# Optimization experiments

Hardware: AMD Instinct MI355X
Metric: run time of the kernel (lower is better)

## Reference

```python
import jax, jax.numpy as jnp
import numpy as np

K = 10        # neighbors
SIGMA = 1.0   # gaussian bandwidth
BIG = 1e9     # diagonal fill so a point is never its own neighbor


def _knn_idx(h, k):
    # h: (B, T, H) -> idx: (B, T, k) of nearest neighbors (euclidean), excluding self
    # squared-distance trick avoids materializing (B, T, T, H)
    sq = jnp.sum(h * h, axis=-1)                                  # (B, T)
    d2 = sq[:, :, None] + sq[:, None, :] - 2.0 * jnp.einsum('bth,bsh->bts', h, h)
    d = jnp.sqrt(jnp.maximum(d2, 0.0))                            # (B, T, T)
    T = h.shape[1]
    eye = jnp.eye(T, dtype=bool)
    d = jnp.where(eye[None, :, :], BIG, d)
    k_eff = min(k, T - 1)
    _, idx = jax.lax.top_k(-d, k_eff)                             # smallest distances
    return idx


def setup_inputs() -> dict:
    key = jax.random.key(0)
    ks = jax.random.split(key, 5)
    B, T, C, H = 64, 1024, 64, 32
    x = jax.random.normal(ks[0], (B, T, C), dtype=jnp.float32)
    s1 = 1.0 / np.sqrt(C)
    s2 = 1.0 / np.sqrt(H)
    W1 = jax.random.uniform(ks[1], (C, H), minval=-s1, maxval=s1, dtype=jnp.float32)
    b1 = jax.random.uniform(ks[2], (H,), minval=-s1, maxval=s1, dtype=jnp.float32)
    W2 = jax.random.uniform(ks[3], (H, H), minval=-s2, maxval=s2, dtype=jnp.float32)
    b2 = jax.random.uniform(ks[4], (H,), minval=-s2, maxval=s2, dtype=jnp.float32)
    return {"x": x, "W1": W1, "b1": b1, "W2": W2, "b2": b2}


def reference(x, W1, b1, W2, b2):
    h = x @ W1 + b1                                               # (B, T, H)
    # kNN graph built under no_grad in the original
    idx = _knn_idx(jax.lax.stop_gradient(h), K)                   # (B, T, k)
    # gather neighbors without the (B, T, T, H) expansion
    neigh = jax.vmap(lambda hb, ib: hb[ib])(h, idx)               # (B, T, k, H)
    diff = neigh - h[:, :, None, :]
    dist = jnp.sqrt(jnp.sum(diff * diff, axis=-1))                # (B, T, k)
    w = jnp.exp(-dist ** 2 / (2.0 * SIGMA ** 2 + 1e-8))
    w = w / (jnp.sum(w, axis=-1, keepdims=True) + 1e-8)
    smooth = jnp.einsum('btk,btkh->bth', w, neigh)                # (B, T, H)
    lap = h - smooth
    return jnp.tanh(lap) @ W2 + b2
```

## Files before the change

### kernel.cpp

```cpp
#include <hip/hip_runtime.h>
#include <math.h>

#define BB 64
#define TT 1024
#define CC 64
#define HH 32
#define KNN 10

typedef float v4f __attribute__((ext_vector_type(4)));
typedef _Float16 f16x8 __attribute__((ext_vector_type(8)));

__device__ __forceinline__ unsigned umn(unsigned a, unsigned b) { return a < b ? a : b; }
__device__ __forceinline__ unsigned umx(unsigned a, unsigned b) { return a > b ? a : b; }

__global__ __launch_bounds__(256) void h_kernel(
    const float* __restrict__ x, const float* __restrict__ W1,
    const float* __restrict__ b1, float* __restrict__ h, float* __restrict__ hsq)
{
    __shared__ float w1s[CC][HH];
    __shared__ float b1s[HH];
    int tid = threadIdx.x;
    for (int i = tid; i < CC * HH; i += 256) w1s[i >> 5][i & 31] = W1[i];
    if (tid < HH) b1s[tid] = b1[tid];
    __syncthreads();

    int row = blockIdx.x * 256 + tid;
    const float4* xr = (const float4*)(x + (size_t)row * CC);
    float acc[HH];
    #pragma unroll
    for (int j = 0; j < HH; ++j) acc[j] = b1s[j];
    #pragma unroll
    for (int c4 = 0; c4 < CC / 4; ++c4) {
        float4 xv = xr[c4];
        #pragma unroll
        for (int j = 0; j < HH; ++j) {
            acc[j] = fmaf(xv.x, w1s[c4 * 4 + 0][j], acc[j]);
            acc[j] = fmaf(xv.y, w1s[c4 * 4 + 1][j], acc[j]);
            acc[j] = fmaf(xv.z, w1s[c4 * 4 + 2][j], acc[j]);
            acc[j] = fmaf(xv.w, w1s[c4 * 4 + 3][j], acc[j]);
        }
    }
    float s = 0.f;
    #pragma unroll
    for (int j = 0; j < HH; ++j) s = fmaf(acc[j], acc[j], s);
    float* hr = h + (size_t)row * HH;
    #pragma unroll
    for (int q = 0; q < HH / 4; ++q) {
        float4 v = { acc[4*q], acc[4*q+1], acc[4*q+2], acc[4*q+3] };
        ((float4*)hr)[q] = v;
    }
    hsq[row] = 0.5f * s * 1048576.0f;
}

#define INSERT_PAIR(kE, kO) do {                                       \
    unsigned lo_ = umn(kE, kO), hi_ = umx(kE, kO);                     \
    bd9 = umn(umn(bd9, umx(bd8, lo_)), umx(bd7, hi_));                 \
    bd8 = umn(umn(bd8, umx(bd7, lo_)), umx(bd6, hi_));                 \
    bd7 = umn(umn(bd7, umx(bd6, lo_)), umx(bd5, hi_));                 \
    bd6 = umn(umn(bd6, umx(bd5, lo_)), umx(bd4, hi_));                 \
    bd5 = umn(umn(bd5, umx(bd4, lo_)), umx(bd3, hi_));                 \
    bd4 = umn(umn(bd4, umx(bd3, lo_)), umx(bd2, hi_));                 \
    bd3 = umn(umn(bd3, umx(bd2, lo_)), umx(bd1, hi_));                 \
    bd2 = umn(umn(bd2, umx(bd1, lo_)), umx(bd0, hi_));                 \
    bd1 = umn(umn(bd1, umx(bd0, lo_)), hi_);                           \
    bd0 = umn(bd0, lo_);                                               \
} while (0)

__global__ __launch_bounds__(512, 8) void lap_kernel(
    const float* __restrict__ h, const float* __restrict__ hsq,
    const float* __restrict__ W2, const float* __restrict__ b2,
    float* __restrict__ out)
{
    __shared__ __align__(16) unsigned char smem[36864];
    auto cah  = reinterpret_cast<_Float16 (*)[2][64][32]>(smem);
    auto cal  = reinterpret_cast<_Float16 (*)[2][64][32]>(smem + 16384);
    float* hsql = reinterpret_cast<float*>(smem + 32768);
    auto s_key  = reinterpret_cast<unsigned (*)[64][KNN]>(smem);
    float* e_wk = reinterpret_cast<float*>(smem + 20480);
    short* e_id = reinterpret_cast<short*>(smem + 23040);
    float* e_inv = reinterpret_cast<float*>(smem + 24320);
    float* w2s  = reinterpret_cast<float*>(smem + 24576);
    float* b2s  = reinterpret_cast<float*>(smem + 28672);
    float* a_pool = reinterpret_cast<float*>(smem);

    int tid  = threadIdx.x;
    int lane = tid & 63;
    int wid  = __builtin_amdgcn_readfirstlane(tid >> 6);

    int g   = blockIdx.x;
    int l   = g >> 3;
    int bb  = ((g & 7) << 3) | (l & 7);
    int rb  = (l >> 3) << 6;

    const float* hb  = h   + (size_t)bb * TT * HH;
    const float* sqb = hsq + (size_t)bb * TT;

    int gtg  = wid & 3;
    int half = wid >> 2;
    int n    = lane & 15;
    int kc   = lane >> 4;

    int trow = rb + gtg * 16 + n;
    f16x8 Bhi, Blo;
    {
        const float* tp = hb + (size_t)trow * HH + kc * 8;
        float4 f1 = ((const float4*)tp)[0];
        float4 f2 = ((const float4*)tp)[1];
        float tf[8] = { f1.x, f1.y, f1.z, f1.w, f2.x, f2.y, f2.z, f2.w };
        #pragma unroll
        for (int e = 0; e < 8; ++e) {
            _Float16 hh = (_Float16)tf[e];
            Bhi[e] = hh;
            Blo[e] = (_Float16)(tf[e] - (float)hh);
        }
    }
    float cinit20 = sqb[trow] + 1048576.0f;

    int s_local = trow - half * 512;
    bool selfok = ((unsigned)s_local < 512u) && (((s_local >> 2) & 3) == kc);
    int self_t7 = selfok ? (((s_local >> 6) << 4) | (((s_local >> 4) & 3) << 2)
                           | (s_local & 3)) : -1;

    unsigned bd0 = 0xFFFFFFFFu, bd1 = 0xFFFFFFFFu, bd2 = 0xFFFFFFFFu,
             bd3 = 0xFFFFFFFFu, bd4 = 0xFFFFFFFFu, bd5 = 0xFFFFFFFFu,
             bd6 = 0xFFFFFFFFu, bd7 = 0xFFFFFFFFu, bd8 = 0xFFFFFFFFu,
             bd9 = 0xFFFFFFFFu;

    int st_c = tid & 3, st_r = (tid >> 2) & 63, st_h = tid >> 8;
    int st_cp = (st_c + (st_r >> 1)) & 3;
    int rd_cp = (kc + (n >> 1)) & 3;

    auto STAGE = [&](int buf, int t) {
        const float* p = hb + (size_t)(st_h * 512 + t * 64 + st_r) * HH + st_c * 8;
        float4 f1 = ((const float4*)p)[0];
        float4 f2 = ((const float4*)p)[1];
        float fe[8] = { f1.x, f1.y, f1.z, f1.w, f2.x, f2.y, f2.z, f2.w };
        f16x8 hi8, lo8;
        #pragma unroll
        for (int e = 0; e < 8; ++e) {
            _Float16 hh = (_Float16)fe[e];
            hi8[e] = hh;
            lo8[e] = (_Float16)(fe[e] - (float)hh);
        }
        *(f16x8*)&cah[buf][st_h][st_r][st_cp * 8] = hi8;
        *(f16x8*)&cal[buf][st_h][st_r][st_cp * 8] = lo8;
    };

    for (int i = tid; i < TT; i += 512) hsql[i] = sqb[i];
    STAGE(0, 0);
    __syncthreads();

    for (int t = 0; t < 8; ++t) {
        if (t < 7) STAGE((t + 1) & 1, t + 1);
        int buf = t & 1;
        #pragma unroll
        for (int sub = 0; sub < 4; ++sub) {
            f16x8 Ahi = *(const f16x8*)&cah[buf][half][sub * 16 + n][rd_cp * 8];
            f16x8 Alo = *(const f16x8*)&cal[buf][half][sub * 16 + n][rd_cp * 8];
            v4f acc = { 0.f, 0.f, 0.f, 0.f };
            acc = __builtin_amdgcn_mfma_f32_16x16x32_f16(Ahi, Bhi, acc, 0, 0, 0);
            acc = __builtin_amdgcn_mfma_f32_16x16x32_f16(Ahi, Blo, acc, 0, 0, 0);
            acc = __builtin_amdgcn_mfma_f32_16x16x32_f16(Alo, Bhi, acc, 0, 0, 0);
            const float4 hv = *(const float4*)&hsql[half * 512 + t * 64
                                                    + sub * 16 + kc * 4];
            int t7b = (t << 4) | (sub << 2);
            float k0f = fmaf(acc[0], -1048576.0f, cinit20 + hv.x);
            float k1f = fmaf(acc[1], -1048576.0f, cinit20 + hv.y);
            float k2f = fmaf(acc[2], -1048576.0f, cinit20 + hv.z);
            float k3f = fmaf(acc[3], -1048576.0f, cinit20 + hv.w);
            unsigned p0 = (umn((unsigned)k0f, 0x1FFFFFFu) << 7) | (unsigned)(t7b + 0);
            unsigned p1 = (umn((unsigned)k1f, 0x1FFFFFFu) << 7) | (unsigned)(t7b + 1);
            unsigned p2 = (umn((unsigned)k2f, 0x1FFFFFFu) << 7) | (unsigned)(t7b + 2);
            unsigned p3 = (umn((unsigned)k3f, 0x1FFFFFFu) << 7) | (unsigned)(t7b + 3);
            p0 = (t7b + 0 == self_t7) ? 0xFFFFFFFFu : p0;
            p1 = (t7b + 1 == self_t7) ? 0xFFFFFFFFu : p1;
            p2 = (t7b + 2 == self_t7) ? 0xFFFFFFFFu : p2;
            p3 = (t7b + 3 == self_t7) ? 0xFFFFFFFFu : p3;
            INSERT_PAIR(p0, p1);
            INSERT_PAIR(p2, p3);
        }
        __syncthreads();
    }

    {
        int p  = half * 4 + kc;
        int tr = gtg * 16 + n;
        s_key[p][tr][0] = bd0; s_key[p][tr][1] = bd1;
        s_key[p][tr][2] = bd2; s_key[p][tr][3] = bd3;
        s_key[p][tr][4] = bd4; s_key[p][tr][5] = bd5;
        s_key[p][tr][6] = bd6; s_key[p][tr][7] = bd7;
        s_key[p][tr][8] = bd8; s_key[p][tr][9] = bd9;
    }
    for (int i = tid; i < HH * HH; i += 512) w2s[i] = W2[i];
    if (tid < HH) b2s[tid] = b2[tid];
    __syncthreads();

    if (wid == 0) {
        unsigned k0 = s_key[0][lane][0], k1 = s_key[1][lane][0];
        unsigned k2 = s_key[2][lane][0], k3 = s_key[3][lane][0];
        unsigned k4 = s_key[4][lane][0], k5 = s_key[5][lane][0];
        unsigned k6 = s_key[6][lane][0], k7 = s_key[7][lane][0];
        int q0=0,q1=0,q2=0,q3=0,q4=0,q5=0,q6=0,q7=0;
        float wsum = 0.f;
        #pragma unroll
        for (int j = 0; j < KNN; ++j) {
            unsigned mn = k0; int c = 0;
            if (k1 < mn) { mn = k1; c = 1; }
            if (k2 < mn) { mn = k2; c = 2; }
            if (k3 < mn) { mn = k3; c = 3; }
            if (k4 < mn) { mn = k4; c = 4; }
            if (k5 < mn) { mn = k5; c = 5; }
            if (k6 < mn) { mn = k6; c = 6; }
            if (k7 < mn) { mn = k7; c = 7; }
            int t7 = (int)(mn & 127u);
            int abs_ = ((c >> 2) << 9) + ((t7 >> 4) << 6) + (((t7 >> 2) & 3) << 4)
                       + ((c & 3) << 2) + (t7 & 3);
            float kf = (float)(mn >> 7) * 9.5367431640625e-07f;
            float wk = expf(1.0f - kf);
            wsum += wk;
            e_id[lane * KNN + j] = (short)abs_;
            e_wk[lane * KNN + j] = wk;
            if      (c == 0) { ++q0; k0 = (q0 < KNN) ? s_key[0][lane][q0] : 0xFFFFFFFFu; }
            else if (c == 1) { ++q1; k1 = (q1 < KNN) ? s_key[1][lane][q1] : 0xFFFFFFFFu; }
            else if (c == 2) { ++q2; k2 = (q2 < KNN) ? s_key[2][lane][q2] : 0xFFFFFFFFu; }
            else if (c == 3) { ++q3; k3 = (q3 < KNN) ? s_key[3][lane][q3] : 0xFFFFFFFFu; }
            else if (c == 4) { ++q4; k4 = (q4 < KNN) ? s_key[4][lane][q4] : 0xFFFFFFFFu; }
            else if (c == 5) { ++q5; k5 = (q5 < KNN) ? s_key[5][lane][q5] : 0xFFFFFFFFu; }
            else if (c == 6) { ++q6; k6 = (q6 < KNN) ? s_key[6][lane][q6] : 0xFFFFFFFFu; }
            else             { ++q7; k7 = (q7 < KNN) ? s_key[7][lane][q7] : 0xFFFFFFFFu; }
        }
        e_inv[lane] = 1.0f / (wsum + 1e-8f);
    }
    __syncthreads();

    {
        int r  = tid >> 3;
        int g2 = (tid & 7) << 2;
        float ax = 0.f, ay = 0.f, az = 0.f, aw = 0.f;
        #pragma unroll
        for (int k = 0; k < KNN; ++k) {
            int idx  = e_id[r * KNN + k];
            float wk = e_wk[r * KNN + k];
            const float4 nv = *(const float4*)(hb + (size_t)idx * HH + g2);
            ax = fmaf(wk, nv.x, ax);
            ay = fmaf(wk, nv.y, ay);
            az = fmaf(wk, nv.z, az);
            aw = fmaf(wk, nv.w, aw);
        }
        float inv = e_inv[r];
        const float4 hv = *(const float4*)(hb + (size_t)(rb + r) * HH + g2);
        float4 av;
        av.x = tanhf(fmaf(-ax, inv, hv.x));
        av.y = tanhf(fmaf(-ay, inv, hv.y));
        av.z = tanhf(fmaf(-az, inv, hv.z));
        av.w = tanhf(fmaf(-aw, inv, hv.w));
        *(float4*)&a_pool[r * 36 + g2] = av;
    }
    __syncthreads();

    int r   = tid >> 3;
    int c0_ = (tid & 7) << 2;
    float o[4];
    #pragma unroll
    for (int u = 0; u < 4; ++u) o[u] = b2s[c0_ + u];
    #pragma unroll
    for (int j = 0; j < HH; ++j) {
        float av = a_pool[r * 36 + j];
        #pragma unroll
        for (int u = 0; u < 4; ++u) o[u] = fmaf(av, w2s[j * HH + c0_ + u], o[u]);
    }
    float* op = out + ((size_t)bb * TT + rb + r) * HH + c0_;
    float4 o1 = { o[0], o[1], o[2], o[3] };
    *((float4*)op) = o1;
}

extern "C" void kernel_launch(void* const* d_in, const int* in_sizes, int n_in,
                              void* d_out, int out_size, void* d_ws, size_t ws_size,
                              hipStream_t stream) {
    const float* x  = (const float*)d_in[0];
    const float* W1 = (const float*)d_in[1];
    const float* b1 = (const float*)d_in[2];
    const float* W2 = (const float*)d_in[3];
    const float* b2 = (const float*)d_in[4];
    float* outp = (float*)d_out;

    float* h   = (float*)d_ws;
    float* hsq = h + (size_t)BB * TT * HH;

    h_kernel<<<(BB * TT) / 256, 256, 0, stream>>>(x, W1, b1, h, hsq);
    lap_kernel<<<BB * (TT / 64), 512, 0, stream>>>(h, hsq, W2, b2, outp);
}
```

Measured before the change: 79.01 us.

## Precompute fp16 hi/lo split in h_kernel and stream MFMA operands from global

The first kernel now writes h as two fp16 planes (hi and residual lo) instead of fp32. The lap kernel therefore no longer converts and stages tiles through double-buffered LDS with per-tile barriers. Each wave instead loads its A fragments straight from global/L2 with a two-step register prefetch, and the tile index encoding is simplified to match. This removes repeated fp32-to-fp16 splitting across the 1024 blocks per batch and most block syncs. The cost is higher L2 traffic per wave with no LDS reuse across waves, plus reconstructing fp32 from hi+lo in the gather phase.

```diff
diff --git a/kernel.cpp b/kernel.cpp
--- a/kernel.cpp
+++ b/kernel.cpp
@@ -9,13 +9,15 @@
 
 typedef float v4f __attribute__((ext_vector_type(4)));
 typedef _Float16 f16x8 __attribute__((ext_vector_type(8)));
+typedef _Float16 f16x4 __attribute__((ext_vector_type(4)));
 
 __device__ __forceinline__ unsigned umn(unsigned a, unsigned b) { return a < b ? a : b; }
 __device__ __forceinline__ unsigned umx(unsigned a, unsigned b) { return a > b ? a : b; }
 
 __global__ __launch_bounds__(256) void h_kernel(
     const float* __restrict__ x, const float* __restrict__ W1,
-    const float* __restrict__ b1, float* __restrict__ h, float* __restrict__ hsq)
+    const float* __restrict__ b1, _Float16* __restrict__ g16hi,
+    _Float16* __restrict__ g16lo, float* __restrict__ hsq)
 {
     __shared__ float w1s[CC][HH];
     __shared__ float b1s[HH];
@@ -43,11 +45,21 @@
     float s = 0.f;
     #pragma unroll
     for (int j = 0; j < HH; ++j) s = fmaf(acc[j], acc[j], s);
-    float* hr = h + (size_t)row * HH;
-    #pragma unroll
-    for (int q = 0; q < HH / 4; ++q) {
-        float4 v = { acc[4*q], acc[4*q+1], acc[4*q+2], acc[4*q+3] };
-        ((float4*)hr)[q] = v;
+
+    _Float16* hp = g16hi + (size_t)row * HH;
+    _Float16* lp = g16lo + (size_t)row * HH;
+    #pragma unroll
+    for (int q = 0; q < 4; ++q) {
+        f16x8 hi8, lo8;
+        #pragma unroll
+        for (int e = 0; e < 8; ++e) {
+            float v = acc[q * 8 + e];
+            _Float16 hh = (_Float16)v;
+            hi8[e] = hh;
+            lo8[e] = (_Float16)(v - (float)hh);
+        }
+        *(f16x8*)&hp[q * 8] = hi8;
+        *(f16x8*)&lp[q * 8] = lo8;
     }
     hsq[row] = 0.5f * s * 1048576.0f;
 }
@@ -66,21 +78,43 @@
     bd0 = umn(bd0, lo_);                                               \
 } while (0)
 
+#define SUBTILE(U, AHI, ALO) do {                                              \
+    v4f acc = { 0.f, 0.f, 0.f, 0.f };                                          \
+    acc = __builtin_amdgcn_mfma_f32_16x16x32_f16(AHI, Bhi, acc, 0, 0, 0);      \
+    acc = __builtin_amdgcn_mfma_f32_16x16x32_f16(AHI, Blo, acc, 0, 0, 0);      \
+    acc = __builtin_amdgcn_mfma_f32_16x16x32_f16(ALO, Bhi, acc, 0, 0, 0);      \
+    const float4 hv = *(const float4*)&hsql[half * 512 + (U) * 16 + kc * 4];   \
+    int t7b = (U) << 2;                                                        \
+    float k0f = fmaf(acc[0], -1048576.0f, cinit20 + hv.x);                     \
+    float k1f = fmaf(acc[1], -1048576.0f, cinit20 + hv.y);                     \
+    float k2f = fmaf(acc[2], -1048576.0f, cinit20 + hv.z);                     \
+    float k3f = fmaf(acc[3], -1048576.0f, cinit20 + hv.w);                     \
+    unsigned p0 = (umn((unsigned)k0f, 0x1FFFFFFu) << 7) | (unsigned)(t7b + 0); \
+    unsigned p1 = (umn((unsigned)k1f, 0x1FFFFFFu) << 7) | (unsigned)(t7b + 1); \
+    unsigned p2 = (umn((unsigned)k2f, 0x1FFFFFFu) << 7) | (unsigned)(t7b + 2); \
+    unsigned p3 = (umn((unsigned)k3f, 0x1FFFFFFu) << 7) | (unsigned)(t7b + 3); \
+    p0 = (t7b + 0 == self_t7) ? 0xFFFFFFFFu : p0;                              \
+    p1 = (t7b + 1 == self_t7) ? 0xFFFFFFFFu : p1;                              \
+    p2 = (t7b + 2 == self_t7) ? 0xFFFFFFFFu : p2;                              \
+    p3 = (t7b + 3 == self_t7) ? 0xFFFFFFFFu : p3;                              \
+    INSERT_PAIR(p0, p1);                                                       \
+    INSERT_PAIR(p2, p3);                                                       \
+} while (0)
+
 __global__ __launch_bounds__(512, 8) void lap_kernel(
-    const float* __restrict__ h, const float* __restrict__ hsq,
+    const _Float16* __restrict__ g16hi, const _Float16* __restrict__ g16lo,
+    const float* __restrict__ hsq,
     const float* __restrict__ W2, const float* __restrict__ b2,
     float* __restrict__ out)
 {
-    __shared__ __align__(16) unsigned char smem[36864];
-    auto cah  = reinterpret_cast<_Float16 (*)[2][64][32]>(smem);
-    auto cal  = reinterpret_cast<_Float16 (*)[2][64][32]>(smem + 16384);
-    float* hsql = reinterpret_cast<float*>(smem + 32768);
+    __shared__ __align__(16) unsigned char smem[32896];
     auto s_key  = reinterpret_cast<unsigned (*)[64][KNN]>(smem);
     float* e_wk = reinterpret_cast<float*>(smem + 20480);
     short* e_id = reinterpret_cast<short*>(smem + 23040);
     float* e_inv = reinterpret_cast<float*>(smem + 24320);
     float* w2s  = reinterpret_cast<float*>(smem + 24576);
     float* b2s  = reinterpret_cast<float*>(smem + 28672);
+    float* hsql = reinterpret_cast<float*>(smem + 28800);
     float* a_pool = reinterpret_cast<float*>(smem);
 
     int tid  = threadIdx.x;
@@ -92,94 +126,50 @@
     int bb  = ((g & 7) << 3) | (l & 7);
     int rb  = (l >> 3) << 6;
 
-    const float* hb  = h   + (size_t)bb * TT * HH;
-    const float* sqb = hsq + (size_t)bb * TT;
+    const _Float16* hbh = g16hi + (size_t)bb * TT * HH;
+    const _Float16* hbl = g16lo + (size_t)bb * TT * HH;
+    const float*    sqb = hsq   + (size_t)bb * TT;
 
     int gtg  = wid & 3;
     int half = wid >> 2;
     int n    = lane & 15;
     int kc   = lane >> 4;
 
+    for (int i = tid; i < TT; i += 512) hsql[i] = sqb[i];
+    for (int i = tid; i < HH * HH; i += 512) w2s[i] = W2[i];
+    if (tid < HH) b2s[tid] = b2[tid];
+
     int trow = rb + gtg * 16 + n;
-    f16x8 Bhi, Blo;
-    {
-        const float* tp = hb + (size_t)trow * HH + kc * 8;
-        float4 f1 = ((const float4*)tp)[0];
-        float4 f2 = ((const float4*)tp)[1];
-        float tf[8] = { f1.x, f1.y, f1.z, f1.w, f2.x, f2.y, f2.z, f2.w };
-        #pragma unroll
-        for (int e = 0; e < 8; ++e) {
-            _Float16 hh = (_Float16)tf[e];
-            Bhi[e] = hh;
-            Blo[e] = (_Float16)(tf[e] - (float)hh);
-        }
-    }
+    f16x8 Bhi = *(const f16x8*)&hbh[(size_t)trow * HH + kc * 8];
+    f16x8 Blo = *(const f16x8*)&hbl[(size_t)trow * HH + kc * 8];
     float cinit20 = sqb[trow] + 1048576.0f;
 
     int s_local = trow - half * 512;
     bool selfok = ((unsigned)s_local < 512u) && (((s_local >> 2) & 3) == kc);
-    int self_t7 = selfok ? (((s_local >> 6) << 4) | (((s_local >> 4) & 3) << 2)
-                           | (s_local & 3)) : -1;
+    int self_t7 = selfok ? (((s_local >> 4) << 2) | (s_local & 3)) : -1;
 
     unsigned bd0 = 0xFFFFFFFFu, bd1 = 0xFFFFFFFFu, bd2 = 0xFFFFFFFFu,
              bd3 = 0xFFFFFFFFu, bd4 = 0xFFFFFFFFu, bd5 = 0xFFFFFFFFu,
              bd6 = 0xFFFFFFFFu, bd7 = 0xFFFFFFFFu, bd8 = 0xFFFFFFFFu,
              bd9 = 0xFFFFFFFFu;
 
-    int st_c = tid & 3, st_r = (tid >> 2) & 63, st_h = tid >> 8;
-    int st_cp = (st_c + (st_r >> 1)) & 3;
-    int rd_cp = (kc + (n >> 1)) & 3;
-
-    auto STAGE = [&](int buf, int t) {
-        const float* p = hb + (size_t)(st_h * 512 + t * 64 + st_r) * HH + st_c * 8;
-        float4 f1 = ((const float4*)p)[0];
-        float4 f2 = ((const float4*)p)[1];
-        float fe[8] = { f1.x, f1.y, f1.z, f1.w, f2.x, f2.y, f2.z, f2.w };
-        f16x8 hi8, lo8;
-        #pragma unroll
-        for (int e = 0; e < 8; ++e) {
-            _Float16 hh = (_Float16)fe[e];
-            hi8[e] = hh;
-            lo8[e] = (_Float16)(fe[e] - (float)hh);
-        }
-        *(f16x8*)&cah[buf][st_h][st_r][st_cp * 8] = hi8;
-        *(f16x8*)&cal[buf][st_h][st_r][st_cp * 8] = lo8;
-    };
-
-    for (int i = tid; i < TT; i += 512) hsql[i] = sqb[i];
-    STAGE(0, 0);
-    __syncthreads();
-
-    for (int t = 0; t < 8; ++t) {
-        if (t < 7) STAGE((t + 1) & 1, t + 1);
-        int buf = t & 1;
-        #pragma unroll
-        for (int sub = 0; sub < 4; ++sub) {
-            f16x8 Ahi = *(const f16x8*)&cah[buf][half][sub * 16 + n][rd_cp * 8];
-            f16x8 Alo = *(const f16x8*)&cal[buf][half][sub * 16 + n][rd_cp * 8];
-            v4f acc = { 0.f, 0.f, 0.f, 0.f };
-            acc = __builtin_amdgcn_mfma_f32_16x16x32_f16(Ahi, Bhi, acc, 0, 0, 0);
-            acc = __builtin_amdgcn_mfma_f32_16x16x32_f16(Ahi, Blo, acc, 0, 0, 0);
-            acc = __builtin_amdgcn_mfma_f32_16x16x32_f16(Alo, Bhi, acc, 0, 0, 0);
-            const float4 hv = *(const float4*)&hsql[half * 512 + t * 64
-                                                    + sub * 16 + kc * 4];
-            int t7b = (t << 4) | (sub << 2);
-            float k0f = fmaf(acc[0], -1048576.0f, cinit20 + hv.x);
-            float k1f = fmaf(acc[1], -1048576.0f, cinit20 + hv.y);
-            float k2f = fmaf(acc[2], -1048576.0f, cinit20 + hv.z);
-            float k3f = fmaf(acc[3], -1048576.0f, cinit20 + hv.w);
-            unsigned p0 = (umn((unsigned)k0f, 0x1FFFFFFu) << 7) | (unsigned)(t7b + 0);
-            unsigned p1 = (umn((unsigned)k1f, 0x1FFFFFFu) << 7) | (unsigned)(t7b + 1);
-            unsigned p2 = (umn((unsigned)k2f, 0x1FFFFFFu) << 7) | (unsigned)(t7b + 2);
-            unsigned p3 = (umn((unsigned)k3f, 0x1FFFFFFu) << 7) | (unsigned)(t7b + 3);
-            p0 = (t7b + 0 == self_t7) ? 0xFFFFFFFFu : p0;
-            p1 = (t7b + 1 == self_t7) ? 0xFFFFFFFFu : p1;
-            p2 = (t7b + 2 == self_t7) ? 0xFFFFFFFFu : p2;
-            p3 = (t7b + 3 == self_t7) ? 0xFFFFFFFFu : p3;
-            INSERT_PAIR(p0, p1);
-            INSERT_PAIR(p2, p3);
-        }
-        __syncthreads();
+    __syncthreads();
+
+    const _Float16* abase_h = hbh + ((size_t)(half * 512) + n) * HH + kc * 8;
+    const _Float16* abase_l = hbl + ((size_t)(half * 512) + n) * HH + kc * 8;
+    #define ALD_H(U) (*(const f16x8*)(abase_h + (size_t)(U) * 16 * HH))
+    #define ALD_L(U) (*(const f16x8*)(abase_l + (size_t)(U) * 16 * HH))
+
+    f16x8 A0h = ALD_H(0), A0l = ALD_L(0);
+    f16x8 A1h = ALD_H(1), A1l = ALD_L(1);
+    for (int u = 0; u < 32; u += 2) {
+        int u2 = (u + 2 < 32) ? u + 2 : 31;
+        int u3 = (u + 3 < 32) ? u + 3 : 31;
+        f16x8 N0h = ALD_H(u2), N0l = ALD_L(u2);
+        f16x8 N1h = ALD_H(u3), N1l = ALD_L(u3);
+        SUBTILE(u,     A0h, A0l);
+        SUBTILE(u + 1, A1h, A1l);
+        A0h = N0h; A0l = N0l; A1h = N1h; A1l = N1l;
     }
 
     {
@@ -191,8 +181,6 @@
         s_key[p][tr][6] = bd6; s_key[p][tr][7] = bd7;
         s_key[p][tr][8] = bd8; s_key[p][tr][9] = bd9;
     }
-    for (int i = tid; i < HH * HH; i += 512) w2s[i] = W2[i];
-    if (tid < HH) b2s[tid] = b2[tid];
     __syncthreads();
 
     if (wid == 0) {
@@ -213,8 +201,8 @@
             if (k6 < mn) { mn = k6; c = 6; }
             if (k7 < mn) { mn = k7; c = 7; }
             int t7 = (int)(mn & 127u);
-            int abs_ = ((c >> 2) << 9) + ((t7 >> 4) << 6) + (((t7 >> 2) & 3) << 4)
-                       + ((c & 3) << 2) + (t7 & 3);
+            int abs_ = ((c >> 2) << 9) + ((t7 >> 2) << 4) + ((c & 3) << 2)
+                       + (t7 & 3);
             float kf = (float)(mn >> 7) * 9.5367431640625e-07f;
             float wk = expf(1.0f - kf);
             wsum += wk;
@@ -241,19 +229,21 @@
         for (int k = 0; k < KNN; ++k) {
             int idx  = e_id[r * KNN + k];
             float wk = e_wk[r * KNN + k];
-            const float4 nv = *(const float4*)(hb + (size_t)idx * HH + g2);
-            ax = fmaf(wk, nv.x, ax);
-            ay = fmaf(wk, nv.y, ay);
-            az = fmaf(wk, nv.z, az);
-            aw = fmaf(wk, nv.w, aw);
+            f16x4 nh = *(const f16x4*)&hbh[(size_t)idx * HH + g2];
+            f16x4 nl = *(const f16x4*)&hbl[(size_t)idx * HH + g2];
+            ax = fmaf(wk, (float)nh[0] + (float)nl[0], ax);
+            ay = fmaf(wk, (float)nh[1] + (float)nl[1], ay);
+            az = fmaf(wk, (float)nh[2] + (float)nl[2], az);
+            aw = fmaf(wk, (float)nh[3] + (float)nl[3], aw);
         }
         float inv = e_inv[r];
-        const float4 hv = *(const float4*)(hb + (size_t)(rb + r) * HH + g2);
+        f16x4 th = *(const f16x4*)&hbh[(size_t)(rb + r) * HH + g2];
+        f16x4 tl = *(const f16x4*)&hbl[(size_t)(rb + r) * HH + g2];
         float4 av;
-        av.x = tanhf(fmaf(-ax, inv, hv.x));
-        av.y = tanhf(fmaf(-ay, inv, hv.y));
-        av.z = tanhf(fmaf(-az, inv, hv.z));
-        av.w = tanhf(fmaf(-aw, inv, hv.w));
+        av.x = tanhf(fmaf(-ax, inv, (float)th[0] + (float)tl[0]));
+        av.y = tanhf(fmaf(-ay, inv, (float)th[1] + (float)tl[1]));
+        av.z = tanhf(fmaf(-az, inv, (float)th[2] + (float)tl[2]));
+        av.w = tanhf(fmaf(-aw, inv, (float)th[3] + (float)tl[3]));
         *(float4*)&a_pool[r * 36 + g2] = av;
     }
     __syncthreads();
@@ -284,9 +274,10 @@
     const float* b2 = (const float*)d_in[4];
     float* outp = (float*)d_out;
 
-    float* h   = (float*)d_ws;
-    float* hsq = h + (size_t)BB * TT * HH;
-
-    h_kernel<<<(BB * TT) / 256, 256, 0, stream>>>(x, W1, b1, h, hsq);
-    lap_kernel<<<BB * (TT / 64), 512, 0, stream>>>(h, hsq, W2, b2, outp);
+    _Float16* g16hi = (_Float16*)d_ws;
+    _Float16* g16lo = g16hi + (size_t)BB * TT * HH;
+    float*    hsq   = (float*)(g16lo + (size_t)BB * TT * HH);
+
+    h_kernel<<<(BB * TT) / 256, 256, 0, stream>>>(x, W1, b1, g16hi, g16lo, hsq);
+    lap_kernel<<<BB * (TT / 64), 512, 0, stream>>>(g16hi, g16lo, hsq, W2, b2, outp);
 }
```

Result: no change. 77.60 us (-1.8%).
